# Performance work log

Measured on AMD Instinct MI355X. Metric: run time of the kernel, lower is better.

Reference implementation:

```python
import jax, jax.numpy as jnp
import numpy as np

B, C, H, W = 1, 32, 128, 512
PAD = 40  # max disparity; output has PAD+1 planes


def setup_inputs() -> dict:
    key = jax.random.key(0)
    k1, k2 = jax.random.split(key)
    input_1 = jax.random.normal(k1, (B, C, H, W), dtype=jnp.float32)
    input_2 = jax.random.normal(k2, (B, C, H, W), dtype=jnp.float32)
    return {"input_1": input_1, "input_2": input_2, "pad_size": PAD}


def reference(input_1, input_2, pad_size):
    # input_1, input_2: [B, C, H, W]; pad_size: python int
    b, c, h, w = input_1.shape
    # left-pad input_2 along W with zeros (matches F.pad(pad=(pad_size,0,0,0)))
    padded = jnp.pad(input_2, ((0, 0), (0, 0), (0, 0), (pad_size, 0)))
    # torch loop: i = pad_size .. 0, appended in that order, so output plane d
    # uses slice starting at i = pad_size - d.
    d_idx = pad_size - jnp.arange(pad_size + 1)          # [D]
    gather_idx = d_idx[:, None] + jnp.arange(w)[None, :]  # [D, W]
    shifted = jnp.take(padded, gather_idx, axis=3)        # [B, C, H, D, W]
    shifted = jnp.moveaxis(shifted, 3, 2)                 # [B, C, D, H, W]
    # elementwise correlation cost volume
    return input_1[:, :, None, :, :] * shifted            # [B, C, D, H, W]
```

## Files before the change

kernel.cpp:

```cpp
#include <hip/hip_runtime.h>

constexpr int C = 32;
constexpr int H = 128;
constexpr int W = 512;
constexpr int PAD = 40;
constexpr int D = PAD + 1;
constexpr int W4 = W / 4;

__global__ __launch_bounds__(256)
void corr1d_kernel(const float* __restrict__ in1,
                   const float* __restrict__ in2,
                   float* __restrict__ out) {
    const int tid = blockIdx.x * blockDim.x + threadIdx.x;
    const int d = blockIdx.y;
    const int c = blockIdx.z;

    const int h  = tid >> 7;
    const int w4 = tid & (W4 - 1);
    const int w  = w4 * 4;

    const float* row1 = in1 + (c * H + h) * W;
    const float* row2 = in2 + (c * H + h) * W;

    const float4 a = *(const float4*)(row1 + w);

    const int base = w - d;
    float b0 = (base     >= 0) ? row2[base    ] : 0.0f;
    float b1 = (base + 1 >= 0) ? row2[base + 1] : 0.0f;
    float b2 = (base + 2 >= 0) ? row2[base + 2] : 0.0f;
    float b3 = (base + 3 >= 0) ? row2[base + 3] : 0.0f;

    float4 r;
    r.x = a.x * b0;
    r.y = a.y * b1;
    r.z = a.z * b2;
    r.w = a.w * b3;

    float4* outv = (float4*)out;
    outv[((c * D + d) * H + h) * W4 + w4] = r;
}

extern "C" void kernel_launch(void* const* d_in, const int* in_sizes, int n_in,
                              void* d_out, int out_size, void* d_ws, size_t ws_size,
                              hipStream_t stream) {
    const float* in1 = (const float*)d_in[0];
    const float* in2 = (const float*)d_in[1];
    float* out = (float*)d_out;

    dim3 block(256);
    dim3 grid((H * W4) / 256, D, C);
    corr1d_kernel<<<grid, block, 0, stream>>>(in1, in2, out);
}
```

Before: 390.9 us.

## Stage input_2 rows in shared memory and loop over all disparities per thread

Each block now loads two rows of both inputs once, caching input_2 in LDS, and then iterates over all 41 disparities, writing one float4 per plane. This removes the repeated global reads of the inputs for every disparity plane and the unaligned scalar loads. In exchange there are fewer blocks with longer per-thread store loops, and parallelism is reduced to 2048 blocks.

```diff
diff --git a/kernel.cpp b/kernel.cpp
--- a/kernel.cpp
+++ b/kernel.cpp
@@ -11,33 +11,53 @@
 void corr1d_kernel(const float* __restrict__ in1,
                    const float* __restrict__ in2,
                    float* __restrict__ out) {
-    const int tid = blockIdx.x * blockDim.x + threadIdx.x;
-    const int d = blockIdx.y;
-    const int c = blockIdx.z;
+    const int c  = blockIdx.y;
+    const int h0 = blockIdx.x * 2;
+    const int t  = threadIdx.x;
+    const int r  = t >> 7;
+    const int w4 = t & (W4 - 1);
+    const int h  = h0 + r;
 
-    const int h  = tid >> 7;
-    const int w4 = tid & (W4 - 1);
-    const int w  = w4 * 4;
+    __shared__ float4 s2[2][W4];
 
-    const float* row1 = in1 + (c * H + h) * W;
-    const float* row2 = in2 + (c * H + h) * W;
+    const float4* in1v = (const float4*)in1;
+    const float4* in2v = (const float4*)in2;
+    const int rowIdx = (c * H + h) * W4;
 
-    const float4 a = *(const float4*)(row1 + w);
-
-    const int base = w - d;
-    float b0 = (base     >= 0) ? row2[base    ] : 0.0f;
-    float b1 = (base + 1 >= 0) ? row2[base + 1] : 0.0f;
-    float b2 = (base + 2 >= 0) ? row2[base + 2] : 0.0f;
-    float b3 = (base + 3 >= 0) ? row2[base + 3] : 0.0f;
-
-    float4 r;
-    r.x = a.x * b0;
-    r.y = a.y * b1;
-    r.z = a.z * b2;
-    r.w = a.w * b3;
+    const float4 a = in1v[rowIdx + w4];
+    s2[r][w4] = in2v[rowIdx + w4];
+    __syncthreads();
 
     float4* outv = (float4*)out;
-    outv[((c * D + d) * H + h) * W4 + w4] = r;
+    const int obase = (c * D * H + h) * W4 + w4;
+
+    const float4 zero4 = make_float4(0.f, 0.f, 0.f, 0.f);
+
+    #pragma unroll
+    for (int d = 0; d <= PAD; ++d) {
+        const int q  = d >> 2;
+        const int rr = d & 3;
+        const int i0 = w4 - q;
+
+        const float4 cur  = (i0     >= 0) ? s2[r][i0]     : zero4;
+        const float4 prev = (i0 - 1 >= 0) ? s2[r][i0 - 1] : zero4;
+
+        float b0, b1, b2, b3;
+        switch (rr) {
+            case 0:  b0 = cur.x;  b1 = cur.y;  b2 = cur.z;  b3 = cur.w; break;
+            case 1:  b0 = prev.w; b1 = cur.x;  b2 = cur.y;  b3 = cur.z; break;
+            case 2:  b0 = prev.z; b1 = prev.w; b2 = cur.x;  b3 = cur.y; break;
+            default: b0 = prev.y; b1 = prev.z; b2 = prev.w; b3 = cur.x; break;
+        }
+
+        float4 res;
+        res.x = a.x * b0;
+        res.y = a.y * b1;
+        res.z = a.z * b2;
+        res.w = a.w * b3;
+
+        outv[obase + d * H * W4] = res;
+    }
 }
 
 extern "C" void kernel_launch(void* const* d_in, const int* in_sizes, int n_in,
@@ -48,6 +68,6 @@
     float* out = (float*)d_out;
 
     dim3 block(256);
-    dim3 grid((H * W4) / 256, D, C);
+    dim3 grid(H / 2, C);
     corr1d_kernel<<<grid, block, 0, stream>>>(in1, in2, out);
 }
```

Result: faster. 346.8 us (-11.3%).
